# Kernel tuning notes

Measured on AMD Instinct MI355X. Metric: run time of the kernel, lower is better.

The kernel has to match this reference:

```python
import jax, jax.numpy as jnp
import numpy as np

B, ORG, L = 128, 4, 2048
C1, C2 = 128, 64
K0, K1, K2 = 7, 5, 3
VQD, VQN = 64, 1024
CARD, NG = 32, 8
EPS = 1e-5


def _conv(x, w, groups=1):
    # 1D conv, stride 1, 'same' padding (k-1)//2, NCH layout, weight (O, I/g, K)
    p = (w.shape[-1] - 1) // 2
    return jax.lax.conv_general_dilated(
        x, w, (1,), [(p, p)],
        dimension_numbers=('NCH', 'OIH', 'NCH'), feature_group_count=groups)


def _tconv(x, w):
    # ConvTranspose1d(stride=1, padding=(k-1)//2) == conv with channel-transposed, spatially flipped kernel
    return _conv(x, jnp.flip(jnp.transpose(w, (1, 0, 2)), -1))


def _gn(x, g, b, groups=NG):
    Bx, C, T = x.shape
    xr = x.reshape(Bx, groups, C // groups, T)
    mu = xr.mean((2, 3), keepdims=True)
    var = xr.var((2, 3), keepdims=True)
    xn = ((xr - mu) * jax.lax.rsqrt(var + EPS)).reshape(Bx, C, T)
    return xn * g[None, :, None] + b[None, :, None]


def setup_inputs() -> dict:
    key = jax.random.key(0)
    ks = iter(jax.random.split(key, 32))
    w = lambda *s: jax.random.normal(next(ks), s, jnp.float32) * 0.05
    ones = lambda n: jnp.ones((n,), jnp.float32)
    zeros = lambda n: jnp.zeros((n,), jnp.float32)
    D = C1 // 2  # ResNeXt bottleneck width
    return dict(
        x=jax.random.normal(next(ks), (B, ORG, L), jnp.float32),
        w0=w(C1, ORG, K0), g0_g=ones(C1), g0_b=zeros(C1),
        wxa=w(D, C1, 1), gxa_g=ones(D), gxa_b=zeros(D),
        wxb=w(D, D // CARD, K1), gxb_g=ones(D), gxb_b=zeros(D),
        wxc=w(C1, D, 1), gxc_g=ones(C1), gxc_b=zeros(C1),
        w2=w(C2, C1, K2), bn2_g=ones(C2), bn2_b=zeros(C2),
        embed_w=jax.random.uniform(next(ks), (VQN, VQD), jnp.float32, -1.0 / VQD, 1.0 / VQD),
        wd2=w(C2, C1, K2), gd2_g=ones(C1), gd2_b=zeros(C1),
        wd1a=w(C1, C1, K1), gd1a_g=ones(C1), gd1a_b=zeros(C1),
        wd1b=w(C1, C1, K1), gd1b_g=ones(C1), gd1b_b=zeros(C1),
        wd0=w(C1, ORG, K0), bd0=zeros(ORG),
    )


def reference(x, w0, g0_g, g0_b, wxa, gxa_g, gxa_b, wxb, gxb_g, gxb_b,
              wxc, gxc_g, gxc_b, w2, bn2_g, bn2_b, embed_w,
              wd2, gd2_g, gd2_b, wd1a, gd1a_g, gd1a_b, wd1b, gd1b_g, gd1b_b,
              wd0, bd0):
    selu = jax.nn.selu

    # ---- encoder ----
    h = selu(_gn(_conv(x, w0), g0_g, g0_b))  # res0

    def resx(h):  # ResNeXt bottleneck, shared weights (module reuses self.resx)
        y = selu(_gn(_conv(h, wxa), gxa_g, gxa_b))
        y = selu(_gn(_conv(y, wxb, groups=CARD), gxb_g, gxb_b))
        y = _gn(_conv(y, wxc), gxc_g, gxc_b)
        return selu(h + y)

    pool = lambda t: t.reshape(t.shape[0], t.shape[1], -1, 2).max(-1)  # MaxPool1d(2)
    h = pool(resx(h))
    h = pool(resx(h))
    # res2: conv + BatchNorm (eval mode, running stats 0/1 -> affine)
    h = _conv(h, w2) * bn2_g[None, :, None] + bn2_b[None, :, None]

    # ---- vector quantization (vqc=True: quantize channel vectors) ----
    Bh, C, T = h.shape  # C == VQD
    Z = jnp.transpose(h, (0, 2, 1)).reshape(-1, VQD)  # [N, vq_dim]
    d = (jnp.sum(Z * Z, 1, keepdims=True) - 2.0 * (Z @ embed_w.T)
         + jnp.sum(embed_w * embed_w, 1)[None, :])  # [N, vq_num] squared L2
    j = jnp.argmin(d, axis=1)
    W_j = embed_w[j]
    commit_loss = jnp.mean(jnp.sum((Z - jax.lax.stop_gradient(W_j)) ** 2, -1))
    vq_loss = jnp.mean(jnp.sum((jax.lax.stop_gradient(Z) - W_j) ** 2, -1))
    hq = jnp.transpose(W_j.reshape(Bh, T, C), (0, 2, 1))  # back to [B, C, T]

    # ---- decoder ----
    up = lambda t: jnp.repeat(t, 2, axis=-1)  # nearest Upsample(x2)

    def deres1(h):  # basic residual block, shared weights (module reuses self.deres1)
        y = selu(_gn(_tconv(h, wd1a), gd1a_g, gd1a_b))
        y = _gn(_tconv(y, wd1b), gd1b_g, gd1b_b)
        return selu(h + y)

    h = selu(_gn(_tconv(hq, wd2), gd2_g, gd2_b))  # deres2
    h = deres1(up(h))
    h = deres1(up(h))
    recon = _tconv(h, wd0) + bd0[None, :, None]  # deres0 (with bias)
    return recon, commit_loss, vq_loss
```

## Files before the change

### kernel.cpp

```cpp
#include <hip/hip_runtime.h>
#include <math.h>

static constexpr int B_   = 128;
static constexpr int ORG_ = 4;
static constexpr int L_   = 2048;
static constexpr int C1_  = 128;
static constexpr int C2_  = 64;
static constexpr int NG_  = 8;
static constexpr int VQD_ = 64;
static constexpr int VQN_ = 1024;
static constexpr long PTS_ = (long)B_ * (L_ / 4);

typedef __attribute__((ext_vector_type(8))) short bf16x8;
typedef __attribute__((ext_vector_type(4))) float f32x4;

__device__ __forceinline__ float selu_f(float x) {
    const float scale = 1.0507009873554805f;
    const float alpha = 1.6732632423543772f;
    return scale * (x > 0.f ? x : alpha * expm1f(x));
}
__device__ __forceinline__ unsigned short f2bf(float x) {
    unsigned u = __float_as_uint(x);
    u = (u + 0x7FFFu + ((u >> 16) & 1u)) >> 16;
    return (unsigned short)u;
}
__device__ __forceinline__ float bf2f(unsigned short u) {
    return __uint_as_float((unsigned)u << 16);
}

__global__ void wprep_kernel(const float* __restrict__ w, float* __restrict__ wT,
                             int CO, int cig, int K, int so, int si, int sk, int koff)
{
    int idx = blockIdx.x * 256 + threadIdx.x;
    int total = cig * K * CO;
    if (idx >= total) return;
    int o = idx % CO;
    int r = idx / CO;
    int i = r / K, k = r % K;
    wT[idx] = w[(long)o * so + (long)i * si + (long)k * sk + koff];
}

__global__ void wprep_mfma_kernel(const float* __restrict__ w, unsigned short* __restrict__ wb)
{
    int idx = blockIdx.x * 256 + threadIdx.x;
    if (idx >= 5 * 16 * 128 * 8) return;
    int j  = idx & 7;
    int o  = (idx >> 3) & 127;
    int kk = idx >> 10;
    int ig = kk & 3, ic = (kk >> 2) & 3, k = kk >> 4;
    int i  = ic * 32 + ig * 8 + j;
    wb[idx] = f2bf(w[(long)i * (128 * 5) + o * 5 + (4 - k)]);
}

__global__ void fill_kernel(float* p, float v, int n)
{
    int i = blockIdx.x * 256 + threadIdx.x;
    if (i < n) p[i] = v;
}

template<int K, int CO, int NTHR, int TT, int OT, int VQ>
__global__ __launch_bounds__(NTHR) void conv_tile_kernel(
    const float* __restrict__ in, const float* __restrict__ wT,
    const float* __restrict__ scale, const float* __restrict__ bias,
    float* __restrict__ out,
    int CI, int T, int cig, int cog,
    const float* __restrict__ ist, const float* __restrict__ ig,
    const float* __restrict__ ibt, int icpg, int iselu,
    const float* __restrict__ res,
    float* __restrict__ vbest, int* __restrict__ vbj, int jbase, long vstride)
{
    constexpr int P    = (K - 1) / 2;
    constexpr int SPAN = TT + K - 1;
    constexpr int RS   = (SPAN + 3) & ~3;
    constexpr int NO   = CO / OT;
    constexpr int NT   = (CO * TT) / (NTHR * OT);
    constexpr int XW   = NT + K - 1;
    extern __shared__ float lds[];

    if constexpr (VQ) {
        const int z = blockIdx.z;
        wT    += (long)z * cig * K * CO;
        bias  += (long)z * CO;
        vbest += (long)z * vstride;
        vbj   += (long)z * vstride;
        jbase += z * CO;
    }

    const int tile = blockIdx.x;
    const int b    = blockIdx.y;
    const int t0g  = tile * TT;
    const float* inb = in + (long)b * CI * T;

    for (int idx = threadIdx.x; idx < CI * SPAN; idx += NTHR) {
        int c = idx / SPAN, j = idx % SPAN;
        int tt = t0g + j - P;
        float v = 0.f;
        if (tt >= 0 && tt < T) {
            v = inb[(long)c * T + tt];
            if (ist) {
                const float* s = &ist[2 * (b * NG_ + c / icpg)];
                v = (v - s[0]) * s[1] * ig[c] + ibt[c];
                if (res) v += res[((long)b * CI + c) * T + tt];
                if (iselu) v = selu_f(v);
            }
        }
        lds[c * RS + j] = v;
    }
    __syncthreads();

    const int o0   = (threadIdx.x % NO) * OT;
    const int slot = threadIdx.x / NO;
    const int t0   = slot * NT;
    const int g    = o0 / cog;
    const float* wrow = wT + o0;

    float acc[OT][NT];
#pragma unroll
    for (int oo = 0; oo < OT; ++oo)
#pragma unroll
        for (int u = 0; u < NT; ++u) acc[oo][u] = 0.f;

    for (int i = 0; i < cig; ++i) {
        const int irow = g * cig + i;
        float xin[(XW + 3) & ~3];
        if constexpr (NT % 4 == 0) {
            constexpr int X4 = (XW + 3) / 4;
            const float4* l4 = reinterpret_cast<const float4*>(&lds[irow * RS + t0]);
#pragma unroll
            for (int j = 0; j < X4; ++j) {
                float4 v = l4[j];
                xin[4 * j]     = v.x;
                xin[4 * j + 1] = v.y;
                xin[4 * j + 2] = v.z;
                xin[4 * j + 3] = v.w;
            }
        } else {
#pragma unroll
            for (int j = 0; j < XW; ++j) xin[j] = lds[irow * RS + t0 + j];
        }
        float wk[OT][K];
#pragma unroll
        for (int oo = 0; oo < OT; ++oo)
#pragma unroll
            for (int k = 0; k < K; ++k) wk[oo][k] = wrow[(i * K + k) * CO + oo];
#pragma unroll
        for (int oo = 0; oo < OT; ++oo)
#pragma unroll
            for (int u = 0; u < NT; ++u)
#pragma unroll
                for (int k = 0; k < K; ++k)
                    acc[oo][u] = fmaf(xin[u + k], wk[oo][k], acc[oo][u]);
    }

    if constexpr (VQ) {
        constexpr int RW = (NO >= 64) ? 64 : 32;
        const int lane = threadIdx.x & 63;
#pragma unroll
        for (int u = 0; u < NT; ++u) {
            float bv = 3.4e38f;
            int bj = 0;
#pragma unroll
            for (int oo = 0; oo < OT; ++oo) {
                const int o = o0 + oo;
                float sv = fmaf(acc[oo][u], scale[o], bias[o]);
                if (sv < bv) { bv = sv; bj = jbase + o; }
            }
#pragma unroll
            for (int off = 1; off < RW; off <<= 1) {
                float v2 = __shfl_xor(bv, off);
                int   j2 = __shfl_xor(bj, off);
                if (v2 < bv || (v2 == bv && j2 < bj)) { bv = v2; bj = j2; }
            }
            if ((lane & (RW - 1)) == 0) {
                long n = (long)b * T + t0g + t0 + u;
                vbest[n] = bv;
                vbj[n]   = bj;
            }
        }
    } else {
#pragma unroll
        for (int oo = 0; oo < OT; ++oo) {
            const int o = o0 + oo;
            const float sc = scale ? scale[o] : 1.f;
            const float bi = bias  ? bias[o]  : 0.f;
            float* ob = out + ((long)b * CO + o) * T + t0g + t0;
#pragma unroll
            for (int u = 0; u < NT; ++u) ob[u] = acc[oo][u] * sc + bi;
        }
    }
}

__global__ __launch_bounds__(256) void conv_epi7_kernel(
    const unsigned short* __restrict__ in, const float* __restrict__ wT,
    float* __restrict__ pbuf, int T, int Bc,
    const float* __restrict__ ist, const float* __restrict__ ig_,
    const float* __restrict__ ibt, int icpg,
    const unsigned short* __restrict__ res)
{
    __shared__ float wlds[32 * 7 * 4];
    __shared__ float rows[4][80];

    const int z   = blockIdx.z;
    const int ci0 = z * 32;

    for (int idx = threadIdx.x; idx < 32 * 7 * 4; idx += 256)
        wlds[idx] = wT[ci0 * 7 * 4 + idx];
    __syncthreads();

    const int wid  = threadIdx.x >> 6;
    const int lane = threadIdx.x & 63;
    const int b    = blockIdx.y;
    const int t0w  = blockIdx.x * 256 + wid * 64;
    const int t    = t0w + lane;
    float* row = rows[wid];
    const long base = (long)b * 128 * T;

    float acc0 = 0.f, acc1 = 0.f, acc2 = 0.f, acc3 = 0.f;

    for (int cc = 0; cc < 32; ++cc) {
        const int ci = ci0 + cc;
        const float* s = &ist[2 * (b * NG_ + ci / icpg)];
        const float mu = s[0], rs = s[1];
        const float gc = ig_[ci], bc = ibt[ci];
        const long cbase = base + (long)ci * T;

        float v = bf2f(in[cbase + t]);
        v = (v - mu) * rs * gc + bc;
        v += bf2f(res[cbase + t]);
        v = selu_f(v);
        row[3 + lane] = v;

        if (lane < 3 || lane >= 61) {
            int th   = (lane < 3) ? (t0w - 3 + lane) : (t0w + 3 + lane);
            int ridx = (lane < 3) ? lane : (lane + 6);
            float h = 0.f;
            if (th >= 0 && th < T) {
                h = bf2f(in[cbase + th]);
                h = (h - mu) * rs * gc + bc;
                h += bf2f(res[cbase + th]);
                h = selu_f(h);
            }
            row[ridx] = h;
        }

        float xin[7];
#pragma unroll
        for (int j = 0; j < 7; ++j) xin[j] = row[lane + j];
#pragma unroll
        for (int k = 0; k < 7; ++k) {
            float4 w4 = *(const float4*)&wlds[(cc * 7 + k) * 4];
            acc0 = fmaf(xin[k], w4.x, acc0);
            acc1 = fmaf(xin[k], w4.y, acc1);
            acc2 = fmaf(xin[k], w4.z, acc2);
            acc3 = fmaf(xin[k], w4.w, acc3);
        }
    }

    const long half = (long)Bc * 4 * T;
    float* pb = pbuf + (long)z * half + ((long)b * 4) * T + t;
    pb[0 * T] = acc0;
    pb[1 * T] = acc1;
    pb[2 * T] = acc2;
    pb[3 * T] = acc3;
}

__global__ void epi_comb_kernel(const float* __restrict__ pbuf,
                                const float* __restrict__ bias,
                                float* __restrict__ out, int T, int Bc, long total)
{
    const long half = (long)Bc * 4 * T;
    for (long idx = blockIdx.x * (long)blockDim.x + threadIdx.x; idx < total;
         idx += (long)gridDim.x * blockDim.x) {
        const int o = (int)((idx / T) & 3);
        float v = ((pbuf[idx] + pbuf[half + idx]) + pbuf[2 * half + idx])
                  + pbuf[3 * half + idx];
        out[idx] = v + bias[o];
    }
}

__global__ __launch_bounds__(256) void conv_mfma5_kernel(
    const unsigned short* __restrict__ in, const unsigned short* __restrict__ wb,
    unsigned short* __restrict__ out, int T,
    const float* __restrict__ ist, const float* __restrict__ ig_,
    const float* __restrict__ ibt, int icpg)
{
    constexpr int SPAN = 68, RSI = 136;
    __shared__ unsigned short xlds[SPAN * RSI];

    const int t0g = blockIdx.x * 64;
    const int b   = blockIdx.y;
    const unsigned short* inb = in + (long)b * 128 * T;

    for (int idx = threadIdx.x; idx < 128 * SPAN; idx += 256) {
        int i = idx / SPAN, j = idx % SPAN;
        int tt = t0g + j - 2;
        unsigned short raw = 0;
        if (tt >= 0 && tt < T) {
            raw = inb[(long)i * T + tt];
            if (ist) {
                const float* s = &ist[2 * (b * NG_ + i / icpg)];
                float v = selu_f((bf2f(raw) - s[0]) * s[1] * ig_[i] + ibt[i]);
                raw = f2bf(v);
            }
        }
        xlds[j * RSI + i] = raw;
    }
    __syncthreads();

    const int lane = threadIdx.x & 63;
    const int wid  = threadIdx.x >> 6;
    const int tw   = wid * 16;
    const int mr   = lane & 15;
    const int kg   = lane >> 4;

    f32x4 acc[8];
#pragma unroll
    for (int ot = 0; ot < 8; ++ot) acc[ot] = (f32x4){0.f, 0.f, 0.f, 0.f};

#pragma unroll
    for (int k = 0; k < 5; ++k) {
#pragma unroll
        for (int ic = 0; ic < 4; ++ic) {
            bf16x8 a = *(const bf16x8*)&xlds[(tw + mr + k) * RSI + ic * 32 + kg * 8];
            const unsigned short* wp = wb + (((k * 16 + ic * 4 + kg) * 128) + mr) * 8;
#pragma unroll
            for (int ot = 0; ot < 8; ++ot) {
                bf16x8 bfr = *(const bf16x8*)(wp + ot * 16 * 8);
                acc[ot] = __builtin_amdgcn_mfma_f32_16x16x32_bf16(a, bfr, acc[ot], 0, 0, 0);
            }
        }
    }

#pragma unroll
    for (int ot = 0; ot < 8; ++ot) {
        int o = ot * 16 + mr;
        ushort4 v;
        v.x = f2bf(acc[ot][0]);
        v.y = f2bf(acc[ot][1]);
        v.z = f2bf(acc[ot][2]);
        v.w = f2bf(acc[ot][3]);
        *(ushort4*)&out[((long)b * 128 + o) * T + t0g + tw + kg * 4] = v;
    }
}

__global__ __launch_bounds__(256) void gn_stats_kernel(
    const float* __restrict__ x, float* __restrict__ stats,
    int C, int T, int G)
{
    const int bg = blockIdx.x;
    const int cpg = C / G;
    const int b = bg / G, g = bg % G;
    const float* base = x + ((long)b * C + (long)g * cpg) * T;
    const long n4 = (long)cpg * T / 4;
    const float4* b4 = (const float4*)base;
    float s = 0.f, ss = 0.f;
    for (long i = threadIdx.x; i < n4; i += blockDim.x) {
        float4 v = b4[i];
        s += v.x + v.y + v.z + v.w;
        ss += v.x * v.x + v.y * v.y + v.z * v.z + v.w * v.w;
    }
#pragma unroll
    for (int off = 32; off; off >>= 1) {
        s  += __shfl_down(s, off);
        ss += __shfl_down(ss, off);
    }
    __shared__ float sh_s[4], sh_ss[4];
    const int wid = threadIdx.x >> 6, lane = threadIdx.x & 63;
    if (lane == 0) { sh_s[wid] = s; sh_ss[wid] = ss; }
    __syncthreads();
    if (threadIdx.x == 0) {
        float S = 0.f, SS = 0.f;
        for (int i = 0; i < 4; ++i) { S += sh_s[i]; SS += sh_ss[i]; }
        float inv_n = 1.f / (float)((long)cpg * T);
        float mu  = S * inv_n;
        float var = SS * inv_n - mu * mu;
        stats[2 * bg]     = mu;
        stats[2 * bg + 1] = rsqrtf(var + 1e-5f);
    }
}

__global__ __launch_bounds__(256) void gn_stats_bf16_kernel(
    const unsigned short* __restrict__ x, float* __restrict__ stats,
    int C, int T, int G)
{
    const int bg = blockIdx.x;
    const int cpg = C / G;
    const int b = bg / G, g = bg % G;
    const unsigned short* base = x + ((long)b * C + (long)g * cpg) * T;
    const long n8 = (long)cpg * T / 8;
    const uint4* b8 = (const uint4*)base;
    float s = 0.f, ss = 0.f;
    for (long i = threadIdx.x; i < n8; i += blockDim.x) {
        uint4 v = b8[i];
        unsigned ws[4] = {v.x, v.y, v.z, v.w};
#pragma unroll
        for (int q = 0; q < 4; ++q) {
            float f0 = __uint_as_float(ws[q] << 16);
            float f1 = __uint_as_float(ws[q] & 0xFFFF0000u);
            s += f0 + f1;
            ss += f0 * f0 + f1 * f1;
        }
    }
#pragma unroll
    for (int off = 32; off; off >>= 1) {
        s  += __shfl_down(s, off);
        ss += __shfl_down(ss, off);
    }
    __shared__ float sh_s[4], sh_ss[4];
    const int wid = threadIdx.x >> 6, lane = threadIdx.x & 63;
    if (lane == 0) { sh_s[wid] = s; sh_ss[wid] = ss; }
    __syncthreads();
    if (threadIdx.x == 0) {
        float S = 0.f, SS = 0.f;
        for (int i = 0; i < 4; ++i) { S += sh_s[i]; SS += sh_ss[i]; }
        float inv_n = 1.f / (float)((long)cpg * T);
        float mu  = S * inv_n;
        float var = SS * inv_n - mu * mu;
        stats[2 * bg]     = mu;
        stats[2 * bg + 1] = rsqrtf(var + 1e-5f);
    }
}

__global__ __launch_bounds__(256) void pool_fused_kernel(
    const float* __restrict__ x, const float* __restrict__ xst,
    const float* __restrict__ xg, const float* __restrict__ xb, int xcpg,
    const float* __restrict__ r, const float* __restrict__ rst,
    const float* __restrict__ rg, const float* __restrict__ rb, int rcpg, int rselu,
    float* __restrict__ out, int C, int Tout, long total)
{
    for (long idx = blockIdx.x * (long)blockDim.x + threadIdx.x; idx < total;
         idx += (long)gridDim.x * blockDim.x) {
        const int to = (int)(idx % Tout);
        const int c  = (int)((idx / Tout) % C);
        const int b  = (int)(idx / ((long)Tout * C));
        const long base = ((long)b * C + c) * (2 * Tout);
        const float* sx = &xst[2 * (b * NG_ + c / xcpg)];
        const float xgc = sx[1] * xg[c], xbc = xb[c] - sx[0] * sx[1] * xg[c];
        float rgc = 1.f, rbc = 0.f;
        if (rst) {
            const float* sr = &rst[2 * (b * NG_ + c / rcpg)];
            rgc = sr[1] * rg[c]; rbc = rb[c] - sr[0] * sr[1] * rg[c];
        }
        float f[2];
#pragma unroll
        for (int q = 0; q < 2; ++q) {
            long t = base + 2 * to + q;
            float rv = r[t] * rgc + rbc;
            if (rst && rselu) rv = selu_f(rv);
            f[q] = selu_f(x[t] * xgc + xbc + rv);
        }
        out[((long)b * C + c) * Tout + to] = fmaxf(f[0], f[1]);
    }
}

template<int INBF>
__global__ __launch_bounds__(256) void up_fused_kernel(
    const void* __restrict__ x_, const float* __restrict__ xst,
    const float* __restrict__ xg, const float* __restrict__ xb, int xcpg,
    const unsigned short* __restrict__ res,
    unsigned short* __restrict__ out, int C, int Tin, long total)
{
    for (long idx = blockIdx.x * (long)blockDim.x + threadIdx.x; idx < total;
         idx += (long)gridDim.x * blockDim.x) {
        const int t = (int)(idx % Tin);
        const int c = (int)((idx / Tin) % C);
        const int b = (int)(idx / ((long)Tin * C));
        const float* s = &xst[2 * (b * NG_ + c / xcpg)];
        float v = INBF ? bf2f(((const unsigned short*)x_)[idx])
                       : ((const float*)x_)[idx];
        v = (v - s[0]) * s[1] * xg[c] + xb[c];
        if (res) v += bf2f(res[idx]);
        v = selu_f(v);
        unsigned short h = f2bf(v);
        unsigned pack = (unsigned)h | ((unsigned)h << 16);
        *(unsigned*)(out + (((long)b * C + c) * Tin + t) * 2) = pack;
    }
}

__global__ void wnorm_kernel(const float* __restrict__ codes, float* __restrict__ wn)
{
    int j = blockIdx.x * 256 + threadIdx.x;
    if (j >= VQN_) return;
    const float* c = codes + (long)j * VQD_;
    float s = 0.f;
#pragma unroll
    for (int i = 0; i < VQD_; ++i) s = fmaf(c[i], c[i], s);
    wn[j] = s;
}

__global__ void vq_combine_kernel(const float* __restrict__ vb, const int* __restrict__ vj,
                                  int* __restrict__ bjs, long stride, int NP)
{
    int n = blockIdx.x * 256 + threadIdx.x;
    if (n >= NP) return;
    float best = vb[n];
    int bj = vj[n];
#pragma unroll
    for (int s = 1; s < 4; ++s) {
        float v = vb[(long)s * stride + n];
        if (v < best) { best = v; bj = vj[(long)s * stride + n]; }
    }
    bjs[n] = bj;
}

__global__ __launch_bounds__(256) void vq_gather_kernel(
    const float* __restrict__ h, const float* __restrict__ codes,
    const int* __restrict__ bjs, float* __restrict__ hq, float* __restrict__ loss,
    int T)
{
    const int n0 = blockIdx.x * 64;
    const int b  = n0 / T;
    const int tb = n0 % T;
    __shared__ int sbj[64];
    if (threadIdx.x < 64) sbj[threadIdx.x] = bjs[n0 + threadIdx.x];
    __syncthreads();

    float l = 0.f;
#pragma unroll
    for (int r = 0; r < (VQD_ * 64) / 256; ++r) {
        int idx = r * 256 + (int)threadIdx.x;
        int c  = idx >> 6, tl = idx & 63;
        float wv = codes[(long)sbj[tl] * VQD_ + c];
        long off = ((long)b * VQD_ + c) * T + tb + tl;
        hq[off] = wv;
        float df = h[off] - wv;
        l = fmaf(df, df, l);
    }
#pragma unroll
    for (int off = 32; off; off >>= 1) l += __shfl_down(l, off);
    if ((threadIdx.x & 63) == 0) atomicAdd(loss, l);
}

__global__ void zero_kernel(float* p) { p[0] = 0.f; }

__global__ void finalize_kernel(const float* __restrict__ loss, float* __restrict__ out,
                                float invNP, long off)
{
    float v = loss[0] * invNP;
    out[off]     = v;
    out[off + 1] = v;
}

static inline int nblk(long total, int thr = 256, long cap = 262144) {
    long b = (total + thr - 1) / thr;
    if (b > cap) b = cap;
    if (b < 1) b = 1;
    return (int)b;
}
static inline int ldsz(int CI, int K, int TT = 64) {
    int span = TT + K - 1;
    int rs = (span + 3) & ~3;
    return CI * rs * 4;
}

struct WT {
    long w0, wxa, wxb, wxc, w2, wd2, wd0, total;
};
static WT wt_offsets() {
    WT o; long p = 0;
    o.w0   = p; p += (long)ORG_ * 7 * C1_;
    o.wxa  = p; p += (long)C1_ * 1 * (C1_ / 2);
    o.wxb  = p; p += 2L * 5 * (C1_ / 2);
    o.wxc  = p; p += (long)(C1_ / 2) * 1 * C1_;
    o.w2   = p; p += (long)C1_ * 3 * C2_;
    o.wd2  = p; p += (long)C2_ * 3 * C1_;
    o.wd0  = p; p += (long)C1_ * 7 * ORG_;
    o.total = p;
    return o;
}

static void run_chunk(const float* x, const float* const* W, const float* wt,
                      const WT& wo, const unsigned short* wbA, const unsigned short* wbB,
                      const float* wn, const float* wts, const float* neg2,
                      float* vbest4, int* vbj4, int* bjs, float* out,
                      float* A, float* Bb, float* Cc, float* st, float* lossbuf,
                      int Bc, long nbuf, hipStream_t stream)
{
    const float* g0_g  = W[1];
    const float* g0_b  = W[2];
    const float* gxa_g = W[4];
    const float* gxa_b = W[5];
    const float* gxb_g = W[7];
    const float* gxb_b = W[8];
    const float* gxc_g = W[10];
    const float* gxc_b = W[11];
    const float* bn2_g = W[13];
    const float* bn2_b = W[14];
    const float* embed = W[15];
    const float* gd2_g = W[17];
    const float* gd2_b = W[18];
    const float* gd1a_g= W[20];
    const float* gd1a_b= W[21];
    const float* gd1b_g= W[23];
    const float* gd1b_b= W[24];
    const float* bd0   = W[26];

    const int D_ = C1_ / 2;
    const int SLOT = 2048;
    float* st0 = st + 0 * SLOT;
    float* st1 = st + 1 * SLOT;
    float* st2 = st + 2 * SLOT;
    float* st3 = st + 3 * SLOT;
    float* st4 = st + 4 * SLOT;
    float* st5 = st + 5 * SLOT;
    float* st6 = st + 6 * SLOT;

    unsigned short* Au  = (unsigned short*)A;
    unsigned short* Bbu = (unsigned short*)Bb;
    unsigned short* Ccu = (unsigned short*)Cc;

    const int nbg = Bc * NG_;
    const int cpg1 = C1_ / NG_;

    int T = L_;

    conv_tile_kernel<7, 128, 512, 64, 1, 0><<<dim3(T / 64, Bc), 512, ldsz(ORG_, 7), stream>>>(
        x, wt + wo.w0, nullptr, nullptr, A, ORG_, T, ORG_, C1_,
        nullptr, nullptr, nullptr, 0, 0, nullptr, nullptr, nullptr, 0, 0);
    gn_stats_kernel<<<nbg, 256, 0, stream>>>(A, st0, C1_, T, NG_);

    conv_tile_kernel<1, 64, 512, 64, 2, 0><<<dim3(T / 64, Bc), 512, ldsz(C1_, 1), stream>>>(
        A, wt + wo.wxa, nullptr, nullptr, Bb, C1_, T, C1_, D_,
        st0, g0_g, g0_b, cpg1, 1, nullptr, nullptr, nullptr, 0, 0);
    gn_stats_kernel<<<nbg, 256, 0, stream>>>(Bb, st1, D_, T, NG_);

    conv_tile_kernel<5, 64, 512, 64, 1, 0><<<dim3(T / 64, Bc), 512, ldsz(D_, 5), stream>>>(
        Bb, wt + wo.wxb, nullptr, nullptr, Bb + nbuf / 2, D_, T, 2, 2,
        st1, gxa_g, gxa_b, D_ / NG_, 1, nullptr, nullptr, nullptr, 0, 0);
    gn_stats_kernel<<<nbg, 256, 0, stream>>>(Bb + nbuf / 2, st2, D_, T, NG_);

    conv_tile_kernel<1, 128, 512, 64, 2, 0><<<dim3(T / 64, Bc), 512, ldsz(D_, 1), stream>>>(
        Bb + nbuf / 2, wt + wo.wxc, nullptr, nullptr, Cc, D_, T, D_, C1_,
        st2, gxb_g, gxb_b, D_ / NG_, 1, nullptr, nullptr, nullptr, 0, 0);
    gn_stats_kernel<<<nbg, 256, 0, stream>>>(Cc, st3, C1_, T, NG_);

    {
        int Tout = T / 2;
        long tt = (long)Bc * C1_ * Tout;
        pool_fused_kernel<<<nblk(tt), 256, 0, stream>>>(
            Cc, st3, gxc_g, gxc_b, cpg1,
            A, st0, g0_g, g0_b, cpg1, 1,
            Bb, C1_, Tout, tt);
        T = Tout;
    }

    conv_tile_kernel<1, 64, 512, 64, 2, 0><<<dim3(T / 64, Bc), 512, ldsz(C1_, 1), stream>>>(
        Bb, wt + wo.wxa, nullptr, nullptr, Cc, C1_, T, C1_, D_,
        nullptr, nullptr, nullptr, 0, 0, nullptr, nullptr, nullptr, 0, 0);
    gn_stats_kernel<<<nbg, 256, 0, stream>>>(Cc, st1, D_, T, NG_);

    conv_tile_kernel<5, 64, 512, 64, 1, 0><<<dim3(T / 64, Bc), 512, ldsz(D_, 5), stream>>>(
        Cc, wt + wo.wxb, nullptr, nullptr, Cc + nbuf / 2, D_, T, 2, 2,
        st1, gxa_g, gxa_b, D_ / NG_, 1, nullptr, nullptr, nullptr, 0, 0);
    gn_stats_kernel<<<nbg, 256, 0, stream>>>(Cc + nbuf / 2, st2, D_, T, NG_);

    conv_tile_kernel<1, 128, 512, 64, 2, 0><<<dim3(T / 64, Bc), 512, ldsz(D_, 1), stream>>>(
        Cc + nbuf / 2, wt + wo.wxc, nullptr, nullptr, A, D_, T, D_, C1_,
        st2, gxb_g, gxb_b, D_ / NG_, 1, nullptr, nullptr, nullptr, 0, 0);
    gn_stats_kernel<<<nbg, 256, 0, stream>>>(A, st3, C1_, T, NG_);

    {
        int Tout = T / 2;
        long tt = (long)Bc * C1_ * Tout;
        pool_fused_kernel<<<nblk(tt), 256, 0, stream>>>(
            A, st3, gxc_g, gxc_b, cpg1,
            Bb, nullptr, nullptr, nullptr, 0, 0,
            Cc, C1_, Tout, tt);
        T = Tout;
    }

    conv_tile_kernel<3, 64, 512, 64, 1, 0><<<dim3(T / 64, Bc), 512, ldsz(C1_, 3), stream>>>(
        Cc, wt + wo.w2, bn2_g, bn2_b, Bb, C1_, T, C1_, C2_,
        nullptr, nullptr, nullptr, 0, 0, nullptr, nullptr, nullptr, 0, 0);

    {
        int NP = Bc * T;
        conv_tile_kernel<1, 256, 512, 64, 8, 1><<<dim3(T / 64, Bc, 4), 512,
                                                  ldsz(VQD_, 1), stream>>>(
            Bb, wts, neg2, wn, nullptr,
            VQD_, T, VQD_, 256,
            nullptr, nullptr, nullptr, 0, 0, nullptr,
            vbest4, vbj4, 0, PTS_);
        vq_combine_kernel<<<(NP + 255) / 256, 256, 0, stream>>>(vbest4, vbj4, bjs, PTS_, NP);
        vq_gather_kernel<<<NP / 64, 256, 0, stream>>>(Bb, embed, bjs, A, lossbuf, T);
    }

    conv_tile_kernel<3, 128, 512, 64, 1, 0><<<dim3(T / 64, Bc), 512, ldsz(C2_, 3), stream>>>(
        A, wt + wo.wd2, nullptr, nullptr, Bb, C2_, T, C2_, C1_,
        nullptr, nullptr, nullptr, 0, 0, nullptr, nullptr, nullptr, 0, 0);
    gn_stats_kernel<<<nbg, 256, 0, stream>>>(Bb, st4, C1_, T, NG_);

    {
        long tt = (long)Bc * C1_ * T;
        up_fused_kernel<0><<<nblk(tt), 256, 0, stream>>>(
            Bb, st4, gd2_g, gd2_b, cpg1, nullptr, Ccu, C1_, T, tt);
        T *= 2;
    }

    conv_mfma5_kernel<<<dim3(T / 64, Bc), 256, 0, stream>>>(
        Ccu, wbA, Au, T, nullptr, nullptr, nullptr, 0);
    gn_stats_bf16_kernel<<<nbg, 256, 0, stream>>>(Au, st5, C1_, T, NG_);

    conv_mfma5_kernel<<<dim3(T / 64, Bc), 256, 0, stream>>>(
        Au, wbB, Bbu, T, st5, gd1a_g, gd1a_b, cpg1);
    gn_stats_bf16_kernel<<<nbg, 256, 0, stream>>>(Bbu, st6, C1_, T, NG_);

    {
        long tt = (long)Bc * C1_ * T;
        up_fused_kernel<1><<<nblk(tt), 256, 0, stream>>>(
            Bbu, st6, gd1b_g, gd1b_b, cpg1, Ccu, Au, C1_, T, tt);
        T *= 2;
    }

    conv_mfma5_kernel<<<dim3(T / 64, Bc), 256, 0, stream>>>(
        Au, wbA, Ccu, T, nullptr, nullptr, nullptr, 0);
    gn_stats_bf16_kernel<<<nbg, 256, 0, stream>>>(Ccu, st5, C1_, T, NG_);

    conv_mfma5_kernel<<<dim3(T / 64, Bc), 256, 0, stream>>>(
        Ccu, wbB, Bbu, T, st5, gd1a_g, gd1a_b, cpg1);
    gn_stats_bf16_kernel<<<nbg, 256, 0, stream>>>(Bbu, st6, C1_, T, NG_);

    {
        float* pbuf = Cc;
        conv_epi7_kernel<<<dim3(T / 256, Bc, 4), 256, 0, stream>>>(
            Bbu, wt + wo.wd0, pbuf, T, Bc,
            st6, gd1b_g, gd1b_b, cpg1, Au);
        long tt = (long)Bc * 4 * T;
        epi_comb_kernel<<<nblk(tt), 256, 0, stream>>>(pbuf, bd0, out, T, Bc, tt);
    }
}

extern "C" void kernel_launch(void* const* d_in, const int* in_sizes, int n_in,
                              void* d_out, int out_size, void* d_ws, size_t ws_size,
                              hipStream_t stream) {
    const float* x = (const float*)d_in[0];
    const float* W[27];
    for (int i = 0; i < 27; ++i) W[i] = (const float*)d_in[i + 1];

    float* out = (float*)d_out;
    const WT wo = wt_offsets();

    const long WT_F32  = 262144;
    const long WB_F32  = 2 * 81920 / 2;
    const long WTS_F32 = VQN_ * VQD_;
    const long ST_F32  = 8 * 2048;
    const long VQ_F32  = 4 * PTS_ + 4 * PTS_ + PTS_;
    const long FIXED = WT_F32 + WB_F32 + 1024 + WTS_F32 + 256 + ST_F32 + 64 + VQ_F32;
    int Bc = 0;
    for (int cand = B_; cand >= 1; cand >>= 1) {
        size_t need = ((size_t)FIXED + (size_t)3 * cand * C1_ * L_) * sizeof(float);
        if (need <= ws_size) { Bc = cand; break; }
    }
    if (Bc == 0) return;

    float* wt            = (float*)d_ws;
    unsigned short* wbA  = (unsigned short*)(wt + WT_F32);
    unsigned short* wbB  = wbA + 81920;
    float* wn            = wt + WT_F32 + WB_F32;
    float* wts           = wn + 1024;
    float* neg2          = wts + WTS_F32;
    float* st            = neg2 + 256;
    float* lossbuf       = st + ST_F32;
    float* vbest4        = lossbuf + 64;
    int*   vbj4          = (int*)(vbest4 + 4 * PTS_);
    int*   bjs           = vbj4 + 4 * PTS_;
    const long nbuf = (long)Bc * C1_ * L_;
    float* A  = (float*)(bjs + PTS_);
    float* Bb = A + nbuf;
    float* Cc = Bb + nbuf;

    const int D_ = C1_ / 2;

    auto prep = [&](const float* w, long off, int CO, int cig, int K,
                    int so, int si, int sk, int koff) {
        int total = cig * K * CO;
        wprep_kernel<<<(total + 255) / 256, 256, 0, stream>>>(
            w, wt + off, CO, cig, K, so, si, sk, koff);
    };
    prep(W[0],  wo.w0,   C1_, ORG_, 7, ORG_ * 7, 7,        1,  0);
    prep(W[3],  wo.wxa,  D_,  C1_,  1, C1_,      1,        1,  0);
    prep(W[6],  wo.wxb,  D_,  2,    5, 2 * 5,    5,        1,  0);
    prep(W[9],  wo.wxc,  C1_, D_,   1, D_,       1,        1,  0);
    prep(W[12], wo.w2,   C2_, C1_,  3, C1_ * 3,  3,        1,  0);
    prep(W[16], wo.wd2,  C1_, C2_,  3, 3,        C1_ * 3, -1,  2);
    prep(W[25], wo.wd0,  ORG_, C1_, 7, 7,        ORG_ * 7, -1, 6);
    wprep_mfma_kernel<<<81920 / 256, 256, 0, stream>>>(W[19], wbA);
    wprep_mfma_kernel<<<81920 / 256, 256, 0, stream>>>(W[22], wbB);
    wnorm_kernel<<<(VQN_ + 255) / 256, 256, 0, stream>>>(W[15], wn);
    for (int q = 0; q < 4; ++q) {
        wprep_kernel<<<(256 * VQD_ + 255) / 256, 256, 0, stream>>>(
            W[15] + (long)q * 256 * VQD_, wts + (long)q * 256 * VQD_,
            256, VQD_, 1, VQD_, 1, 1, 0);
    }
    fill_kernel<<<1, 256, 0, stream>>>(neg2, -2.f, 256);

    zero_kernel<<<1, 1, 0, stream>>>(lossbuf);

    for (int b0 = 0; b0 < B_; b0 += Bc) {
        const float* xc = x + (long)b0 * ORG_ * L_;
        float* outc = out + (long)b0 * ORG_ * L_;
        run_chunk(xc, W, wt, wo, wbA, wbB, wn, wts, neg2, vbest4, vbj4, bjs,
                  outc, A, Bb, Cc, st, lossbuf, Bc, nbuf, stream);
    }

    {
        float invNP = 1.f / (float)(B_ * (L_ / 4));
        finalize_kernel<<<1, 1, 0, stream>>>(lossbuf, out, invNP, (long)out_size - 2);
    }
}
```

Measured before the change: 2.097 ms.

## Enlarge conv_mfma5 time tile to 256 so each wave reuses weight fragments

The MFMA conv kernel now covers 256 time steps per block instead of 64. Each wave computes four 16-row M tiles, so every weight fragment loaded from global memory feeds four MFMAs instead of one, and the halo overhead in shared memory shrinks relative to the tile. In exchange, the per-thread accumulator array grows to 128 floats, which may lower occupancy. Shared memory grows to about 70KB per block, and the grid has fewer blocks.

```diff
diff --git a/kernel.cpp b/kernel.cpp
--- a/kernel.cpp
+++ b/kernel.cpp
@@ -284,10 +284,10 @@
     const float* __restrict__ ist, const float* __restrict__ ig_,
     const float* __restrict__ ibt, int icpg)
 {
-    constexpr int SPAN = 68, RSI = 136;
+    constexpr int TTm = 256, SPAN = 260, RSI = 136;
     __shared__ unsigned short xlds[SPAN * RSI];
 
-    const int t0g = blockIdx.x * 64;
+    const int t0g = blockIdx.x * TTm;
     const int b   = blockIdx.y;
     const unsigned short* inb = in + (long)b * 128 * T;
 
@@ -309,37 +309,47 @@
 
     const int lane = threadIdx.x & 63;
     const int wid  = threadIdx.x >> 6;
-    const int tw   = wid * 16;
+    const int tw   = wid * 64;
     const int mr   = lane & 15;
     const int kg   = lane >> 4;
 
-    f32x4 acc[8];
-#pragma unroll
-    for (int ot = 0; ot < 8; ++ot) acc[ot] = (f32x4){0.f, 0.f, 0.f, 0.f};
+    f32x4 acc[4][8];
+#pragma unroll
+    for (int m = 0; m < 4; ++m)
+#pragma unroll
+        for (int ot = 0; ot < 8; ++ot) acc[m][ot] = (f32x4){0.f, 0.f, 0.f, 0.f};
 
 #pragma unroll
     for (int k = 0; k < 5; ++k) {
 #pragma unroll
         for (int ic = 0; ic < 4; ++ic) {
-            bf16x8 a = *(const bf16x8*)&xlds[(tw + mr + k) * RSI + ic * 32 + kg * 8];
+            bf16x8 a[4];
+#pragma unroll
+            for (int m = 0; m < 4; ++m)
+                a[m] = *(const bf16x8*)&xlds[(tw + m * 16 + mr + k) * RSI + ic * 32 + kg * 8];
             const unsigned short* wp = wb + (((k * 16 + ic * 4 + kg) * 128) + mr) * 8;
 #pragma unroll
             for (int ot = 0; ot < 8; ++ot) {
                 bf16x8 bfr = *(const bf16x8*)(wp + ot * 16 * 8);
-                acc[ot] = __builtin_amdgcn_mfma_f32_16x16x32_bf16(a, bfr, acc[ot], 0, 0, 0);
+#pragma unroll
+                for (int m = 0; m < 4; ++m)
+                    acc[m][ot] = __builtin_amdgcn_mfma_f32_16x16x32_bf16(a[m], bfr, acc[m][ot], 0, 0, 0);
             }
         }
     }
 
 #pragma unroll
-    for (int ot = 0; ot < 8; ++ot) {
-        int o = ot * 16 + mr;
-        ushort4 v;
-        v.x = f2bf(acc[ot][0]);
-        v.y = f2bf(acc[ot][1]);
-        v.z = f2bf(acc[ot][2]);
-        v.w = f2bf(acc[ot][3]);
-        *(ushort4*)&out[((long)b * 128 + o) * T + t0g + tw + kg * 4] = v;
+    for (int m = 0; m < 4; ++m) {
+#pragma unroll
+        for (int ot = 0; ot < 8; ++ot) {
+            int o = ot * 16 + mr;
+            ushort4 v;
+            v.x = f2bf(acc[m][ot][0]);
+            v.y = f2bf(acc[m][ot][1]);
+            v.z = f2bf(acc[m][ot][2]);
+            v.w = f2bf(acc[m][ot][3]);
+            *(ushort4*)&out[((long)b * 128 + o) * T + t0g + tw + m * 16 + kg * 4] = v;
+        }
     }
 }
 
@@ -697,11 +707,11 @@
         T *= 2;
     }
 
-    conv_mfma5_kernel<<<dim3(T / 64, Bc), 256, 0, stream>>>(
+    conv_mfma5_kernel<<<dim3(T / 256, Bc), 256, 0, stream>>>(
         Ccu, wbA, Au, T, nullptr, nullptr, nullptr, 0);
     gn_stats_bf16_kernel<<<nbg, 256, 0, stream>>>(Au, st5, C1_, T, NG_);
 
-    conv_mfma5_kernel<<<dim3(T / 64, Bc), 256, 0, stream>>>(
+    conv_mfma5_kernel<<<dim3(T / 256, Bc), 256, 0, stream>>>(
         Au, wbB, Bbu, T, st5, gd1a_g, gd1a_b, cpg1);
     gn_stats_bf16_kernel<<<nbg, 256, 0, stream>>>(Bbu, st6, C1_, T, NG_);
 
@@ -712,11 +722,11 @@
         T *= 2;
     }
 
-    conv_mfma5_kernel<<<dim3(T / 64, Bc), 256, 0, stream>>>(
+    conv_mfma5_kernel<<<dim3(T / 256, Bc), 256, 0, stream>>>(
         Au, wbA, Ccu, T, nullptr, nullptr, nullptr, 0);
     gn_stats_bf16_kernel<<<nbg, 256, 0, stream>>>(Ccu, st5, C1_, T, NG_);
 
-    conv_mfma5_kernel<<<dim3(T / 64, Bc), 256, 0, stream>>>(
+    conv_mfma5_kernel<<<dim3(T / 256, Bc), 256, 0, stream>>>(
         Ccu, wbB, Bbu, T, st5, gd1a_g, gd1a_b, cpg1);
     gn_stats_bf16_kernel<<<nbg, 256, 0, stream>>>(Bbu, st6, C1_, T, NG_);
 
```

After: 2.338 ms. 1.11x slower.
